# Performance work log

Measured on AMD Instinct MI355X. Metric: run time of the kernel, lower is better.

Reference implementation:

```python
import jax, jax.numpy as jnp
import numpy as np

T, B, F = 2048, 2, 1024
H = 16
DK = F // H


def setup_inputs() -> dict:
    key = jax.random.key(0)
    ks = jax.random.split(key, 13)
    s = 0.02
    return {
        "query": jax.random.normal(ks[0], (T, B, F), jnp.float32),
        "key": jax.random.normal(ks[1], (T, B, F), jnp.float32),
        "value": jax.random.normal(ks[2], (T, B, F), jnp.float32),
        "key_padding_mask": jax.random.randint(ks[3], (B, T), 0, 2).astype(bool),
        "Wq": jax.random.normal(ks[4], (F, F), jnp.float32) * s,
        "bq": jnp.zeros((F,), jnp.float32),
        "Wk": jax.random.normal(ks[5], (F, F), jnp.float32) * s,
        "bk": jnp.zeros((F,), jnp.float32),
        "Wv": jax.random.normal(ks[6], (F, F), jnp.float32) * s,
        "bv": jnp.zeros((F,), jnp.float32),
        "Wo": jax.random.normal(ks[7], (F, F), jnp.float32) * s,
        "bo": jnp.zeros((F,), jnp.float32),
    }


def reference(query, key, value, key_padding_mask, Wq, bq, Wk, bk, Wv, bv, Wo, bo):
    # inputs are [T, B, F]; module transposes to batch-major [B, T, F]
    q = jnp.swapaxes(query, 0, 1)
    k = jnp.swapaxes(key, 0, 1)
    v = jnp.swapaxes(value, 0, 1)
    nb = q.shape[0]
    # QKV projections, split into heads: [B, H, T, DK]
    def proj(x, W, b):
        y = x @ W.T + b
        return y.reshape(nb, -1, H, DK).transpose(0, 2, 1, 3)
    qh, kh, vh = proj(q, Wq, bq), proj(k, Wk, bk), proj(v, Wv, bv)
    # scores [B, H, Tq, Tk]
    scores = jnp.einsum("bhqd,bhkd->bhqk", qh, kh) / jnp.sqrt(jnp.float32(DK))
    scores = jnp.where(key_padding_mask[:, None, None, :], -jnp.inf, scores)
    attn = jax.nn.softmax(scores, axis=-1)
    # AV + merge heads + out proj (dropout p=0 -> identity)
    ctx = jnp.einsum("bhqk,bhkd->bhqd", attn, vh)
    ctx = ctx.transpose(0, 2, 1, 3).reshape(nb, -1, H * DK)
    out = ctx @ Wo.T + bo
    return jnp.swapaxes(out, 0, 1)  # back to [T, B, F]
```

## Files before the change

kernel.cpp:

```cpp
#include <hip/hip_runtime.h>
#include <hip/hip_bf16.h>
#include <stdint.h>


typedef __bf16 bf16_t;
typedef __bf16 bf16x4 __attribute__((ext_vector_type(4)));
typedef __bf16 bf16x8 __attribute__((ext_vector_type(8)));
typedef float f32x4 __attribute__((ext_vector_type(4)));
typedef unsigned int u32x2 __attribute__((ext_vector_type(2)));

typedef const __attribute__((address_space(1))) void* gas_ptr;
typedef __attribute__((address_space(3))) void* las_ptr;

__device__ __forceinline__ void gload16(const void* g, void* lds) {
    __builtin_amdgcn_global_load_lds((gas_ptr)g, (las_ptr)lds, 16, 0, 0);
}

__device__ __forceinline__ int swz(int o) { return o ^ (((o >> 7) & 7) << 4); }

__device__ __forceinline__ int gofs(int c) {
    return ((c >> 5) << 9) + (((c >> 1) & 3) << 7) + (((c >> 3) & 3) << 5) + ((c & 1) << 4);
}

#define TRREAD(dst, addr, IMM) \
    asm volatile("ds_read_b64_tr_b16 %0, %1 offset:" #IMM : "=v"(dst) : "v"(addr))

#if __has_builtin(__builtin_amdgcn_exp2f)
#define EXP2F(x) __builtin_amdgcn_exp2f(x)
#else
#define EXP2F(x) exp2f(x)
#endif
#if __has_builtin(__builtin_amdgcn_rcpf)
#define RCPF(x) __builtin_amdgcn_rcpf(x)
#else
#define RCPF(x) (1.0f / (x))
#endif

__global__ __launch_bounds__(256) void prep_all_kernel(const float* __restrict__ q,
                                                       const float* __restrict__ k,
                                                       const float* __restrict__ v,
                                                       const float* __restrict__ wq,
                                                       const float* __restrict__ wk,
                                                       const float* __restrict__ wv,
                                                       const float* __restrict__ wo,
                                                       const unsigned char* __restrict__ mraw,
                                                       bf16_t* __restrict__ xdst,
                                                       bf16_t* __restrict__ wdst,
                                                       unsigned long long* __restrict__ mbits) {
    const int bidx = blockIdx.x;
    const int tid = threadIdx.x;
    if (bidx < 6144) {
        int idx = bidx * 256 + tid;
        int which = idx >> 19;
        int loc = idx & 524287;
        const float* src = which == 0 ? q : which == 1 ? k : v;
        int e0 = loc * 8;
        int t = e0 >> 11, r = e0 & 2047, b = r >> 10, f = r & 1023;
        const float4* s = (const float4*)(src + e0);
        float4 a = s[0], c = s[1];
        bf16x8 o;
        o[0] = (bf16_t)a.x; o[1] = (bf16_t)a.y; o[2] = (bf16_t)a.z; o[3] = (bf16_t)a.w;
        o[4] = (bf16_t)c.x; o[5] = (bf16_t)c.y; o[6] = (bf16_t)c.z; o[7] = (bf16_t)c.w;
        *(bf16x8*)(xdst + (size_t)which * 4194304 + ((size_t)b * 2048 + t) * 1024 + f) = o;
    } else if (bidx < 8192) {
        int idx = (bidx - 6144) * 256 + tid;
        int which = idx >> 17;
        int loc = idx & 131071;
        const float* src = which == 0 ? wq : which == 1 ? wk : which == 2 ? wv : wo;
        int e0 = loc * 8;
        const float4* s = (const float4*)(src + e0);
        float4 a = s[0], c = s[1];
        bf16x8 o;
        o[0] = (bf16_t)a.x; o[1] = (bf16_t)a.y; o[2] = (bf16_t)a.z; o[3] = (bf16_t)a.w;
        o[4] = (bf16_t)c.x; o[5] = (bf16_t)c.y; o[6] = (bf16_t)c.z; o[7] = (bf16_t)c.w;
        *(bf16x8*)(wdst + (size_t)which * 1048576 + e0) = o;
    } else {
        __shared__ int s_isbyte;
        if (tid == 0) s_isbyte = 0;
        __syncthreads();
        int any = 0;
        for (int i = tid; i < 4096; i += 256)
            if ((i & 3) && mraw[i]) any = 1;
        if (any) atomicOr(&s_isbyte, 1);
        __syncthreads();
        if (tid < 64) {
            int b = tid >> 5, kt = tid & 31;
            unsigned long long bits = 0;
            if (s_isbyte) {
                for (int j = 0; j < 64; ++j)
                    if (mraw[b * 2048 + kt * 64 + j]) bits |= 1ull << j;
            } else {
                const int* ri = (const int*)mraw;
                for (int j = 0; j < 64; ++j)
                    if (ri[b * 2048 + kt * 64 + j]) bits |= 1ull << j;
            }
            mbits[tid] = bits;
        }
    }
}

__global__ __launch_bounds__(256) void gemm_kernel(const bf16_t* __restrict__ A0,
                                                   const bf16_t* __restrict__ Bw0,
                                                   const float* __restrict__ b0,
                                                   const float* __restrict__ b1,
                                                   const float* __restrict__ b2,
                                                   bf16_t* __restrict__ outb,
                                                   float* __restrict__ outf,
                                                   int mode) {
    __shared__ __align__(16) bf16_t Asm[128 * 32];
    __shared__ __align__(16) bf16_t Bsm[128 * 32];
    const int tid = threadIdx.x;
    const int wave = tid >> 6, lane = tid & 63;
    const int g = lane >> 4, lr = lane & 15;
    const int z = blockIdx.z;
    const bf16_t* A  = A0 + (size_t)z * 4194304;
    const bf16_t* Bw = Bw0 + (size_t)z * 1048576;
    const float* bias = z == 0 ? b0 : z == 1 ? b1 : b2;
    const float qsc = (mode == 0 && z == 0) ? 0.18033688f : 1.0f;
    const int m0 = blockIdx.y * 128, n0 = blockIdx.x * 128;
    const int wm = (wave >> 1) * 64, wn = (wave & 1) * 64;
    const int srow = wave * 32 + (lane >> 2);
    const int scol = (lane & 3) * 8;

    f32x4 acc[4][4] = {};

    for (int k0 = 0; k0 < 1024; k0 += 32) {
        __syncthreads();
        gload16(A  + (size_t)(m0 + srow) * 1024 + k0 + scol,      (char*)Asm + wave * 2048);
        gload16(A  + (size_t)(m0 + srow + 16) * 1024 + k0 + scol, (char*)Asm + wave * 2048 + 1024);
        gload16(Bw + (size_t)(n0 + srow) * 1024 + k0 + scol,      (char*)Bsm + wave * 2048);
        gload16(Bw + (size_t)(n0 + srow + 16) * 1024 + k0 + scol, (char*)Bsm + wave * 2048 + 1024);
        __syncthreads();

        bf16x8 af[4], bfr[4];
        #pragma unroll
        for (int mi = 0; mi < 4; ++mi)
            af[mi] = *(const bf16x8*)(Asm + (wm + mi * 16 + lr) * 32 + g * 8);
        #pragma unroll
        for (int ni = 0; ni < 4; ++ni)
            bfr[ni] = *(const bf16x8*)(Bsm + (wn + ni * 16 + lr) * 32 + g * 8);
        #pragma unroll
        for (int mi = 0; mi < 4; ++mi)
            #pragma unroll
            for (int ni = 0; ni < 4; ++ni)
                acc[mi][ni] = __builtin_amdgcn_mfma_f32_16x16x32_bf16(af[mi], bfr[ni], acc[mi][ni], 0, 0, 0);
    }

    #pragma unroll
    for (int mi = 0; mi < 4; ++mi) {
        #pragma unroll
        for (int ni = 0; ni < 4; ++ni) {
            int n = n0 + wn + ni * 16 + lr;
            float bs = bias[n];
            #pragma unroll
            for (int i = 0; i < 4; ++i) {
                int m = m0 + wm + mi * 16 + 4 * g + i;
                float v = (acc[mi][ni][i] + bs) * qsc;
                int b = m >> 11, t = m & 2047;
                if (mode == 0) {
                    int hh = n >> 6, dk = n & 63;
                    outb[(size_t)z * 4194304 + ((size_t)(b * 16 + hh) * 2048 + t) * 64 + dk] = (bf16_t)v;
                } else {
                    outf[(size_t)t * 2048 + b * 1024 + n] = v;
                }
            }
        }
    }
}

__global__ __launch_bounds__(256, 2) void attn_kernel(const bf16_t* __restrict__ qh,
                                                      const bf16_t* __restrict__ kh,
                                                      const bf16_t* __restrict__ vh,
                                                      const unsigned long long* __restrict__ mbits,
                                                      bf16_t* __restrict__ ctx) {
    __shared__ __align__(16) bf16_t Ks[2][64 * 64];
    __shared__ __align__(16) bf16_t Vs[2][64 * 64];

    const int tid = threadIdx.x;
    const int wave = tid >> 6, lane = tid & 63;
    const int g = lane >> 4, lr = lane & 15;
    const int bid = blockIdx.x;
    const int sid = (bid & 7) * 64 + (bid >> 3);
    const int bh = sid >> 4, qc = sid & 15;
    const int b = bh >> 4, h = bh & 15;
    const int q0 = qc * 128;
    const bf16_t* Qg = qh + ((size_t)bh * 2048 + q0) * 64;
    const bf16_t* Kg = kh + (size_t)bh * 2048 * 64;
    const bf16_t* Vg = vh + (size_t)bh * 2048 * 64;
    const unsigned long long* mbp = mbits + b * 32;

    const int dstw = wave * 2048;
    const int dl = dstw + lane * 16;
    const int wq0 = wave * 32;
    const int vs0 = gofs(wave * 128 + lane);
    const int vs1 = gofs(wave * 128 + 64 + lane);

    #pragma unroll
    for (int c = 0; c < 4; ++c)
        gload16((const char*)Qg + swz(wave * 4096 + c * 1024 + lane * 16),
                (char*)Ks + wave * 4096 + c * 1024);
    __syncthreads();
    bf16x8 qf[2][2];
    #pragma unroll
    for (int s = 0; s < 2; ++s) {
        qf[s][0] = *(const bf16x8*)((const char*)Ks + swz((wq0 + s * 16 + lr) * 128 + g * 16));
        qf[s][1] = *(const bf16x8*)((const char*)Ks + swz((wq0 + s * 16 + lr) * 128 + 64 + g * 16));
    }
    __syncthreads();

    gload16((const char*)Kg + swz(dl),        (char*)Ks[0] + dstw);
    gload16((const char*)Kg + swz(dl + 1024), (char*)Ks[0] + dstw + 1024);
    gload16((const char*)Vg + vs0,            (char*)Vs[0] + dstw);
    gload16((const char*)Vg + vs1,            (char*)Vs[0] + dstw + 1024);

    bf16x8 ones;
    #pragma unroll
    for (int j = 0; j < 8; ++j) ones[j] = (bf16_t)1.0f;

    f32x4 cacc[2][4] = {};
    f32x4 sacc[2] = {};
    const unsigned vbase = (unsigned)(unsigned long long)(las_ptr)&Vs[0][0] + g * 512 + lr * 8;

    for (int kt = 0; kt < 32; ++kt) {
        const int cur = kt & 1;
        __syncthreads();
        const unsigned long long mb = mbp[kt];

        const int nx = (kt < 31) ? kt + 1 : 31;
        const char* Kn = (const char*)(Kg + nx * 4096);
        const char* Vn = (const char*)(Vg + nx * 4096);
        gload16(Kn + swz(dl),        (char*)Ks[cur ^ 1] + dstw);
        gload16(Kn + swz(dl + 1024), (char*)Ks[cur ^ 1] + dstw + 1024);
        gload16(Vn + vs0,            (char*)Vs[cur ^ 1] + dstw);
        gload16(Vn + vs1,            (char*)Vs[cur ^ 1] + dstw + 1024);

        const char* Kc = (const char*)Ks[cur];
        f32x4 s2[2][4];
        __builtin_amdgcn_s_setprio(1);
        #pragma unroll
        for (int st = 0; st < 4; ++st) {
            bf16x8 kf0 = *(const bf16x8*)(Kc + swz((st * 16 + lr) * 128 + g * 16));
            bf16x8 kf1 = *(const bf16x8*)(Kc + swz((st * 16 + lr) * 128 + 64 + g * 16));
            #pragma unroll
            for (int s = 0; s < 2; ++s) {
                f32x4 zz = {};
                zz = __builtin_amdgcn_mfma_f32_16x16x32_bf16(kf0, qf[s][0], zz, 0, 0, 0);
                zz = __builtin_amdgcn_mfma_f32_16x16x32_bf16(kf1, qf[s][1], zz, 0, 0, 0);
                s2[s][st] = zz;
            }
        }
        __builtin_amdgcn_s_setprio(0);

        const unsigned long long mq = mb >> (4 * g);
        const unsigned mlo = (unsigned)mq, mhi = (unsigned)(mq >> 32);
        #pragma unroll
        for (int st = 0; st < 4; ++st) {
            #pragma unroll
            for (int i = 0; i < 4; ++i) {
                const bool mk = ((st < 2 ? mlo >> (16 * st + i) : mhi >> (16 * (st - 2) + i)) & 1);
                s2[0][st][i] = mk ? 0.f : EXP2F(s2[0][st][i]);
                s2[1][st][i] = mk ? 0.f : EXP2F(s2[1][st][i]);
            }
        }
        bf16x8 pb[2][2];
        #pragma unroll
        for (int s = 0; s < 2; ++s)
            #pragma unroll
            for (int kk = 0; kk < 2; ++kk)
                #pragma unroll
                for (int j = 0; j < 8; ++j)
                    pb[s][kk][j] = (bf16_t)s2[s][2 * kk + (j >> 2)][j & 3];

        const unsigned vb = vbase + (cur ? 8192u : 0u);
        u32x2 t[2][2][4];
        TRREAD(t[0][0][0], vb, 0);    TRREAD(t[0][0][1], vb, 128);
        TRREAD(t[0][0][2], vb, 256);  TRREAD(t[0][0][3], vb, 384);
        TRREAD(t[0][1][0], vb, 2048); TRREAD(t[0][1][1], vb, 2176);
        TRREAD(t[0][1][2], vb, 2304); TRREAD(t[0][1][3], vb, 2432);
        TRREAD(t[1][0][0], vb, 4096); TRREAD(t[1][0][1], vb, 4224);
        TRREAD(t[1][0][2], vb, 4352); TRREAD(t[1][0][3], vb, 4480);
        TRREAD(t[1][1][0], vb, 6144); TRREAD(t[1][1][1], vb, 6272);
        TRREAD(t[1][1][2], vb, 6400); TRREAD(t[1][1][3], vb, 6528);
        asm volatile("s_waitcnt lgkmcnt(0)" ::: "memory");
        __builtin_amdgcn_sched_barrier(0);
        __builtin_amdgcn_s_setprio(1);
        #pragma unroll
        for (int kk = 0; kk < 2; ++kk) {
            sacc[0] = __builtin_amdgcn_mfma_f32_16x16x32_bf16(ones, pb[0][kk], sacc[0], 0, 0, 0);
            sacc[1] = __builtin_amdgcn_mfma_f32_16x16x32_bf16(ones, pb[1][kk], sacc[1], 0, 0, 0);
            #pragma unroll
            for (int ni = 0; ni < 4; ++ni) {
                union { u32x2 q[2]; bf16x8 v8; } u;
                u.q[0] = t[kk][0][ni];
                u.q[1] = t[kk][1][ni];
                #pragma unroll
                for (int s = 0; s < 2; ++s)
                    cacc[s][ni] = __builtin_amdgcn_mfma_f32_16x16x32_bf16(u.v8, pb[s][kk], cacc[s][ni], 0, 0, 0);
            }
        }
        __builtin_amdgcn_s_setprio(0);
    }

    #pragma unroll
    for (int s = 0; s < 2; ++s) {
        const float rl = RCPF(sacc[s][0]);
        const int trow = q0 + wq0 + s * 16 + lr;
        #pragma unroll
        for (int ni = 0; ni < 4; ++ni) {
            bf16x4 o;
            #pragma unroll
            for (int i = 0; i < 4; ++i)
                o[i] = (bf16_t)(cacc[s][ni][i] * rl);
            *(bf16x4*)(ctx + ((size_t)b * 2048 + trow) * 1024 + h * 64 + ni * 16 + 4 * g) = o;
        }
    }
}

extern "C" void kernel_launch(void* const* d_in, const int* in_sizes, int n_in,
                              void* d_out, int out_size, void* d_ws, size_t ws_size,
                              hipStream_t stream) {
    const float* query = (const float*)d_in[0];
    const float* key_  = (const float*)d_in[1];
    const float* value = (const float*)d_in[2];
    const unsigned char* kpm_raw = (const unsigned char*)d_in[3];
    const float* Wq = (const float*)d_in[4];
    const float* bq = (const float*)d_in[5];
    const float* Wk = (const float*)d_in[6];
    const float* bk = (const float*)d_in[7];
    const float* Wv = (const float*)d_in[8];
    const float* bv = (const float*)d_in[9];
    const float* Wo = (const float*)d_in[10];
    const float* bo = (const float*)d_in[11];
    float* out = (float*)d_out;

    char* ws = (char*)d_ws;
    size_t off = 0;
    auto alloc = [&](size_t bytes) {
        char* p = ws + off;
        off += (bytes + 255) & ~(size_t)255;
        return p;
    };
    const size_t SZ_X = (size_t)4096 * 1024 * sizeof(bf16_t);
    const size_t SZ_W = (size_t)1024 * 1024 * sizeof(bf16_t);
    bf16_t* xq  = (bf16_t*)alloc(SZ_X);
    bf16_t* xk  = (bf16_t*)alloc(SZ_X);
    bf16_t* xv  = (bf16_t*)alloc(SZ_X);
    bf16_t* wqb = (bf16_t*)alloc(SZ_W);
    bf16_t* wkb = (bf16_t*)alloc(SZ_W);
    bf16_t* wvb = (bf16_t*)alloc(SZ_W);
    bf16_t* wob = (bf16_t*)alloc(SZ_W);
    bf16_t* qhB = (bf16_t*)alloc(SZ_X);
    bf16_t* khB = (bf16_t*)alloc(SZ_X);
    bf16_t* vhB = (bf16_t*)alloc(SZ_X);
    bf16_t* ctxB = (bf16_t*)alloc(SZ_X);
    unsigned long long* mbits = (unsigned long long*)alloc(64 * sizeof(unsigned long long));
    (void)xk; (void)xv; (void)wkb; (void)wvb;

    prep_all_kernel<<<8193, 256, 0, stream>>>(query, key_, value, Wq, Wk, Wv, Wo,
                                              kpm_raw, xq, wqb, mbits);

    gemm_kernel<<<dim3(8, 32, 3), 256, 0, stream>>>(xq, wqb, bq, bk, bv, qhB, nullptr, 0);

    attn_kernel<<<512, 256, 0, stream>>>(qhB, khB, vhB, mbits, ctxB);

    gemm_kernel<<<dim3(8, 32, 1), 256, 0, stream>>>(ctxB, wob, bo, bo, bo, nullptr, out, 1);
}
```

Measured before the change: 144.9 us.

## Process two KV tiles per barrier iteration in attention kernel

Doubles the shared-memory K/V staging so each main-loop iteration loads and computes two 64-key tiles, halving the number of block-wide barriers and prefetch rounds. The prefetch for the next pair is issued at the start of each iteration. In exchange, LDS use doubles to 64 KB per block, which may reduce occupancy against the launch bound of two blocks per CU. Register pressure also rises because scores for two tiles are kept live at once.

```diff
diff --git a/kernel.cpp b/kernel.cpp
--- a/kernel.cpp
+++ b/kernel.cpp
@@ -173,8 +173,8 @@
                                                       const bf16_t* __restrict__ vh,
                                                       const unsigned long long* __restrict__ mbits,
                                                       bf16_t* __restrict__ ctx) {
-    __shared__ __align__(16) bf16_t Ks[2][64 * 64];
-    __shared__ __align__(16) bf16_t Vs[2][64 * 64];
+    __shared__ __align__(16) bf16_t Ks[2][2][64 * 64];
+    __shared__ __align__(16) bf16_t Vs[2][2][64 * 64];
 
     const int tid = threadIdx.x;
     const int wave = tid >> 6, lane = tid & 63;
@@ -198,20 +198,25 @@
     #pragma unroll
     for (int c = 0; c < 4; ++c)
         gload16((const char*)Qg + swz(wave * 4096 + c * 1024 + lane * 16),
-                (char*)Ks + wave * 4096 + c * 1024);
+                (char*)Ks[0] + wave * 4096 + c * 1024);
     __syncthreads();
     bf16x8 qf[2][2];
     #pragma unroll
     for (int s = 0; s < 2; ++s) {
-        qf[s][0] = *(const bf16x8*)((const char*)Ks + swz((wq0 + s * 16 + lr) * 128 + g * 16));
-        qf[s][1] = *(const bf16x8*)((const char*)Ks + swz((wq0 + s * 16 + lr) * 128 + 64 + g * 16));
+        qf[s][0] = *(const bf16x8*)((const char*)Ks[0] + swz((wq0 + s * 16 + lr) * 128 + g * 16));
+        qf[s][1] = *(const bf16x8*)((const char*)Ks[0] + swz((wq0 + s * 16 + lr) * 128 + 64 + g * 16));
     }
     __syncthreads();
 
-    gload16((const char*)Kg + swz(dl),        (char*)Ks[0] + dstw);
-    gload16((const char*)Kg + swz(dl + 1024), (char*)Ks[0] + dstw + 1024);
-    gload16((const char*)Vg + vs0,            (char*)Vs[0] + dstw);
-    gload16((const char*)Vg + vs1,            (char*)Vs[0] + dstw + 1024);
+    #pragma unroll
+    for (int u = 0; u < 2; ++u) {
+        const char* Kt = (const char*)(Kg + u * 4096);
+        const char* Vt = (const char*)(Vg + u * 4096);
+        gload16(Kt + swz(dl),        (char*)Ks[0][u] + dstw);
+        gload16(Kt + swz(dl + 1024), (char*)Ks[0][u] + dstw + 1024);
+        gload16(Vt + vs0,            (char*)Vs[0][u] + dstw);
+        gload16(Vt + vs1,            (char*)Vs[0][u] + dstw + 1024);
+    }
 
     bf16x8 ones;
     #pragma unroll
@@ -219,86 +224,97 @@
 
     f32x4 cacc[2][4] = {};
     f32x4 sacc[2] = {};
-    const unsigned vbase = (unsigned)(unsigned long long)(las_ptr)&Vs[0][0] + g * 512 + lr * 8;
-
-    for (int kt = 0; kt < 32; ++kt) {
-        const int cur = kt & 1;
-        __syncthreads();
-        const unsigned long long mb = mbp[kt];
-
-        const int nx = (kt < 31) ? kt + 1 : 31;
-        const char* Kn = (const char*)(Kg + nx * 4096);
-        const char* Vn = (const char*)(Vg + nx * 4096);
-        gload16(Kn + swz(dl),        (char*)Ks[cur ^ 1] + dstw);
-        gload16(Kn + swz(dl + 1024), (char*)Ks[cur ^ 1] + dstw + 1024);
-        gload16(Vn + vs0,            (char*)Vs[cur ^ 1] + dstw);
-        gload16(Vn + vs1,            (char*)Vs[cur ^ 1] + dstw + 1024);
-
-        const char* Kc = (const char*)Ks[cur];
-        f32x4 s2[2][4];
+    const unsigned vbase = (unsigned)(unsigned long long)(las_ptr)&Vs[0][0][0] + g * 512 + lr * 8;
+
+    for (int m = 0; m < 16; ++m) {
+        const int par = m & 1;
+        __syncthreads();
+        const unsigned long long mb0 = mbp[2 * m];
+        const unsigned long long mb1 = mbp[2 * m + 1];
+
+        if (m < 15) {
+            #pragma unroll
+            for (int u = 0; u < 2; ++u) {
+                const char* Kn = (const char*)(Kg + (2 * m + 2 + u) * 4096);
+                const char* Vn = (const char*)(Vg + (2 * m + 2 + u) * 4096);
+                gload16(Kn + swz(dl),        (char*)Ks[par ^ 1][u] + dstw);
+                gload16(Kn + swz(dl + 1024), (char*)Ks[par ^ 1][u] + dstw + 1024);
+                gload16(Vn + vs0,            (char*)Vs[par ^ 1][u] + dstw);
+                gload16(Vn + vs1,            (char*)Vs[par ^ 1][u] + dstw + 1024);
+            }
+        }
+
+        f32x4 s2[2][2][4];
         __builtin_amdgcn_s_setprio(1);
         #pragma unroll
-        for (int st = 0; st < 4; ++st) {
-            bf16x8 kf0 = *(const bf16x8*)(Kc + swz((st * 16 + lr) * 128 + g * 16));
-            bf16x8 kf1 = *(const bf16x8*)(Kc + swz((st * 16 + lr) * 128 + 64 + g * 16));
-            #pragma unroll
-            for (int s = 0; s < 2; ++s) {
-                f32x4 zz = {};
-                zz = __builtin_amdgcn_mfma_f32_16x16x32_bf16(kf0, qf[s][0], zz, 0, 0, 0);
-                zz = __builtin_amdgcn_mfma_f32_16x16x32_bf16(kf1, qf[s][1], zz, 0, 0, 0);
-                s2[s][st] = zz;
+        for (int u = 0; u < 2; ++u) {
+            const char* Kc = (const char*)Ks[par][u];
+            #pragma unroll
+            for (int st = 0; st < 4; ++st) {
+                bf16x8 kf0 = *(const bf16x8*)(Kc + swz((st * 16 + lr) * 128 + g * 16));
+                bf16x8 kf1 = *(const bf16x8*)(Kc + swz((st * 16 + lr) * 128 + 64 + g * 16));
+                #pragma unroll
+                for (int s = 0; s < 2; ++s) {
+                    f32x4 zz = {};
+                    zz = __builtin_amdgcn_mfma_f32_16x16x32_bf16(kf0, qf[s][0], zz, 0, 0, 0);
+                    zz = __builtin_amdgcn_mfma_f32_16x16x32_bf16(kf1, qf[s][1], zz, 0, 0, 0);
+                    s2[u][s][st] = zz;
+                }
             }
         }
         __builtin_amdgcn_s_setprio(0);
 
-        const unsigned long long mq = mb >> (4 * g);
-        const unsigned mlo = (unsigned)mq, mhi = (unsigned)(mq >> 32);
-        #pragma unroll
-        for (int st = 0; st < 4; ++st) {
-            #pragma unroll
-            for (int i = 0; i < 4; ++i) {
-                const bool mk = ((st < 2 ? mlo >> (16 * st + i) : mhi >> (16 * (st - 2) + i)) & 1);
-                s2[0][st][i] = mk ? 0.f : EXP2F(s2[0][st][i]);
-                s2[1][st][i] = mk ? 0.f : EXP2F(s2[1][st][i]);
-            }
-        }
-        bf16x8 pb[2][2];
-        #pragma unroll
-        for (int s = 0; s < 2; ++s)
-            #pragma unroll
-            for (int kk = 0; kk < 2; ++kk)
+        #pragma unroll
+        for (int u = 0; u < 2; ++u) {
+            const unsigned long long mq = (u ? mb1 : mb0) >> (4 * g);
+            const unsigned mlo = (unsigned)mq, mhi = (unsigned)(mq >> 32);
+            #pragma unroll
+            for (int st = 0; st < 4; ++st) {
                 #pragma unroll
-                for (int j = 0; j < 8; ++j)
-                    pb[s][kk][j] = (bf16_t)s2[s][2 * kk + (j >> 2)][j & 3];
-
-        const unsigned vb = vbase + (cur ? 8192u : 0u);
-        u32x2 t[2][2][4];
-        TRREAD(t[0][0][0], vb, 0);    TRREAD(t[0][0][1], vb, 128);
-        TRREAD(t[0][0][2], vb, 256);  TRREAD(t[0][0][3], vb, 384);
-        TRREAD(t[0][1][0], vb, 2048); TRREAD(t[0][1][1], vb, 2176);
-        TRREAD(t[0][1][2], vb, 2304); TRREAD(t[0][1][3], vb, 2432);
-        TRREAD(t[1][0][0], vb, 4096); TRREAD(t[1][0][1], vb, 4224);
-        TRREAD(t[1][0][2], vb, 4352); TRREAD(t[1][0][3], vb, 4480);
-        TRREAD(t[1][1][0], vb, 6144); TRREAD(t[1][1][1], vb, 6272);
-        TRREAD(t[1][1][2], vb, 6400); TRREAD(t[1][1][3], vb, 6528);
-        asm volatile("s_waitcnt lgkmcnt(0)" ::: "memory");
-        __builtin_amdgcn_sched_barrier(0);
-        __builtin_amdgcn_s_setprio(1);
-        #pragma unroll
-        for (int kk = 0; kk < 2; ++kk) {
-            sacc[0] = __builtin_amdgcn_mfma_f32_16x16x32_bf16(ones, pb[0][kk], sacc[0], 0, 0, 0);
-            sacc[1] = __builtin_amdgcn_mfma_f32_16x16x32_bf16(ones, pb[1][kk], sacc[1], 0, 0, 0);
-            #pragma unroll
-            for (int ni = 0; ni < 4; ++ni) {
-                union { u32x2 q[2]; bf16x8 v8; } u;
-                u.q[0] = t[kk][0][ni];
-                u.q[1] = t[kk][1][ni];
+                for (int i = 0; i < 4; ++i) {
+                    const bool mk = ((st < 2 ? mlo >> (16 * st + i) : mhi >> (16 * (st - 2) + i)) & 1);
+                    s2[u][0][st][i] = mk ? 0.f : EXP2F(s2[u][0][st][i]);
+                    s2[u][1][st][i] = mk ? 0.f : EXP2F(s2[u][1][st][i]);
+                }
+            }
+            bf16x8 pb[2][2];
+            #pragma unroll
+            for (int s = 0; s < 2; ++s)
                 #pragma unroll
-                for (int s = 0; s < 2; ++s)
-                    cacc[s][ni] = __builtin_amdgcn_mfma_f32_16x16x32_bf16(u.v8, pb[s][kk], cacc[s][ni], 0, 0, 0);
-            }
-        }
-        __builtin_amdgcn_s_setprio(0);
+                for (int kk = 0; kk < 2; ++kk)
+                    #pragma unroll
+                    for (int j = 0; j < 8; ++j)
+                        pb[s][kk][j] = (bf16_t)s2[u][s][2 * kk + (j >> 2)][j & 3];
+
+            const unsigned vb = vbase + (unsigned)par * 16384u + (unsigned)u * 8192u;
+            u32x2 t[2][2][4];
+            TRREAD(t[0][0][0], vb, 0);    TRREAD(t[0][0][1], vb, 128);
+            TRREAD(t[0][0][2], vb, 256);  TRREAD(t[0][0][3], vb, 384);
+            TRREAD(t[0][1][0], vb, 2048); TRREAD(t[0][1][1], vb, 2176);
+            TRREAD(t[0][1][2], vb, 2304); TRREAD(t[0][1][3], vb, 2432);
+            TRREAD(t[1][0][0], vb, 4096); TRREAD(t[1][0][1], vb, 4224);
+            TRREAD(t[1][0][2], vb, 4352); TRREAD(t[1][0][3], vb, 4480);
+            TRREAD(t[1][1][0], vb, 6144); TRREAD(t[1][1][1], vb, 6272);
+            TRREAD(t[1][1][2], vb, 6400); TRREAD(t[1][1][3], vb, 6528);
+            asm volatile("s_waitcnt lgkmcnt(0)" ::: "memory");
+            __builtin_amdgcn_sched_barrier(0);
+            __builtin_amdgcn_s_setprio(1);
+            #pragma unroll
+            for (int kk = 0; kk < 2; ++kk) {
+                sacc[0] = __builtin_amdgcn_mfma_f32_16x16x32_bf16(ones, pb[0][kk], sacc[0], 0, 0, 0);
+                sacc[1] = __builtin_amdgcn_mfma_f32_16x16x32_bf16(ones, pb[1][kk], sacc[1], 0, 0, 0);
+                #pragma unroll
+                for (int ni = 0; ni < 4; ++ni) {
+                    union { u32x2 q[2]; bf16x8 v8; } uu;
+                    uu.q[0] = t[kk][0][ni];
+                    uu.q[1] = t[kk][1][ni];
+                    #pragma unroll
+                    for (int s = 0; s < 2; ++s)
+                        cacc[s][ni] = __builtin_amdgcn_mfma_f32_16x16x32_bf16(uu.v8, pb[s][kk], cacc[s][ni], 0, 0, 0);
+                }
+            }
+            __builtin_amdgcn_s_setprio(0);
+        }
     }
 
     #pragma unroll
```

New measurement: 139.8 us. 3.5% less time.
